# Optimization experiments

Hardware: AMD Instinct MI355X
Metric: run time of the kernel (lower is better)

Reference implementation:

```python
import jax, jax.numpy as jnp
import numpy as np

B, N, E = 16, 4096, 2_000_000
STRENGTH = 1.0
RADIAL_CUTOFF = 3.0
EPS = 1e-8


def setup_inputs() -> dict:
    key = jax.random.key(0)
    k0, k1, k2, k3, k4, k5, k6 = jax.random.split(key, 7)
    relative_coordinates = jax.random.uniform(k0, (B, N, 3), dtype=jnp.float32)
    # well-conditioned unit cells: ~10 Angstrom box with small perturbation
    basis_vectors = 10.0 * jnp.eye(3, dtype=jnp.float32)[None] \
        + 0.3 * jax.random.normal(k1, (B, 3, 3), dtype=jnp.float32)
    src = jax.random.randint(k2, (E,), 0, N)
    dst = jax.random.randint(k3, (E,), 0, N)
    bch = jax.random.randint(k4, (E,), 0, B)
    shifts = 0.5 * jax.random.normal(k5, (E, 3), dtype=jnp.float32)
    raw_scores_X = jax.random.normal(k6, (B, N, 3), dtype=jnp.float32)
    return {
        "relative_coordinates": relative_coordinates,
        "basis_vectors": basis_vectors,
        "shifts": shifts,
        "raw_scores_X": raw_scores_X,
        "src": src,
        "dst": dst,
        "bch": bch,
    }


def reference(relative_coordinates, basis_vectors, shifts, raw_scores_X, src, dst, bch):
    # cartesian positions: rel coords expressed in the basis-vector rows
    pos = jnp.einsum("bni,bij->bnj", relative_coordinates, basis_vectors)  # [B,N,3]
    # per-edge cartesian displacements (gather)
    disp = pos[bch, dst] - pos[bch, src] + shifts  # [E,3]
    r = jnp.linalg.norm(disp, axis=1)  # [E]
    # F(r) prefactor: 2 s (r - r0) / (r + eps)
    prefactor = 2.0 * STRENGTH * (r - RADIAL_CUTOFF) / (r + EPS)
    contributions = prefactor[:, None] * disp  # [E,3]
    # scatter-add edge contributions onto source nodes
    node_idx = N * bch + src
    cart_forces = jax.ops.segment_sum(contributions, node_idx, num_segments=B * N)
    cart_forces = cart_forces.reshape(B, N, 3)
    # back to relative coordinates via reciprocal basis (inverse of basis)
    reciprocal = jnp.linalg.inv(basis_vectors)  # [B,3,3]
    rel_forces = jnp.einsum("bni,bij->bnj", cart_forces, reciprocal)
    # augmented X-score: raw score + repulsive pseudo-force
    return raw_scores_X + rel_forces
```

## Files before the change

kernel.cpp:

```cpp
#include <hip/hip_runtime.h>

#define NBLK 1024
#define NBUK 16
#define NQ   4
#define QSH  10
#define NBUCK (NBUK * NQ)
#define MAXN 4096
#define SCAN_N (NBUCK * NBLK)
#define SCAN_BS 1024
#define MAXPPB 16

__global__ void prep_kernel(const float* __restrict__ rel,
                            const float* __restrict__ basis,
                            const int* __restrict__ src,
                            const int* __restrict__ bch,
                            float4* __restrict__ pos4,
                            int* __restrict__ ghist,
                            int BN, int N, int E, int chunk, int PB) {
    int blk = blockIdx.x, tid = threadIdx.x;
    if (blk < PB) {
        int idx = blk * 256 + tid;
        if (idx < BN) {
            int b = idx / N;
            const float* bm = basis + b * 9;
            float x = rel[idx * 3 + 0], y = rel[idx * 3 + 1], z = rel[idx * 3 + 2];
            float4 p;
            p.x = x * bm[0] + y * bm[3] + z * bm[6];
            p.y = x * bm[1] + y * bm[4] + z * bm[7];
            p.z = x * bm[2] + y * bm[5] + z * bm[8];
            p.w = 0.0f;
            pos4[idx] = p;
        }
        return;
    }
    __shared__ int h[NBUCK];
    int hb = blk - PB;
    if (tid < NBUCK) h[tid] = 0;
    __syncthreads();
    int lo = hb * chunk, hi = min(E, lo + chunk);
    for (int e0 = lo + tid * 8; e0 < hi; e0 += 2048) {
        if (e0 + 7 < hi) {
            int4 bA = *(const int4*)(bch + e0);
            int4 bB = *(const int4*)(bch + e0 + 4);
            int4 sA = *(const int4*)(src + e0);
            int4 sB = *(const int4*)(src + e0 + 4);
            atomicAdd(&h[bA.x * NQ + (sA.x >> QSH)], 1);
            atomicAdd(&h[bA.y * NQ + (sA.y >> QSH)], 1);
            atomicAdd(&h[bA.z * NQ + (sA.z >> QSH)], 1);
            atomicAdd(&h[bA.w * NQ + (sA.w >> QSH)], 1);
            atomicAdd(&h[bB.x * NQ + (sB.x >> QSH)], 1);
            atomicAdd(&h[bB.y * NQ + (sB.y >> QSH)], 1);
            atomicAdd(&h[bB.z * NQ + (sB.z >> QSH)], 1);
            atomicAdd(&h[bB.w * NQ + (sB.w >> QSH)], 1);
        } else {
            for (int e = e0; e < hi; ++e)
                atomicAdd(&h[bch[e] * NQ + (src[e] >> QSH)], 1);
        }
    }
    __syncthreads();
    if (tid < NBUCK) ghist[tid * NBLK + hb] = h[tid];
}

__global__ void scan1_kernel(int* __restrict__ g, int* __restrict__ bsums) {
    __shared__ int tp[256];
    int tid = threadIdx.x;
    int base = blockIdx.x * SCAN_BS + tid * 4;
    int v0 = g[base], v1 = g[base + 1], v2 = g[base + 2], v3 = g[base + 3];
    int s = v0 + v1 + v2 + v3;
    tp[tid] = s;
    for (int off = 1; off < 256; off <<= 1) {
        __syncthreads();
        int t = (tid >= off) ? tp[tid - off] : 0;
        __syncthreads();
        tp[tid] += t;
    }
    __syncthreads();
    int incl = tp[tid];
    int excl = incl - s;
    g[base]     = excl;
    g[base + 1] = excl + v0;
    g[base + 2] = excl + v0 + v1;
    g[base + 3] = excl + v0 + v1 + v2;
    if (tid == 255) bsums[blockIdx.x] = incl;
}

__global__ void scan2_kernel(int* __restrict__ bsums, int n) {
    __shared__ int tp[1024];
    int tid = threadIdx.x;
    int v = (tid < n) ? bsums[tid] : 0;
    tp[tid] = v;
    for (int off = 1; off < 1024; off <<= 1) {
        __syncthreads();
        int t = (tid >= off) ? tp[tid - off] : 0;
        __syncthreads();
        tp[tid] += t;
    }
    __syncthreads();
    if (tid < n) bsums[tid] = tp[tid] - v;
}

__global__ void scatter_kernel(const float* __restrict__ shifts,
                               const int* __restrict__ src,
                               const int* __restrict__ dst,
                               const int* __restrict__ bch,
                               const int* __restrict__ ghist,
                               const int* __restrict__ bsums,
                               float4* __restrict__ recs,
                               int E, int chunk) {
    __shared__ int cur[NBUCK];
    int tid = threadIdx.x, blk = blockIdx.x;
    if (tid < NBUCK) {
        int idx = tid * NBLK + blk;
        cur[tid] = ghist[idx] + bsums[idx >> 10];
    }
    __syncthreads();
    int lo = blk * chunk, hi = min(E, lo + chunk);
    for (int e0 = lo + tid * 8; e0 < hi; e0 += 2048) {
        if (e0 + 7 < hi) {
            int4 sA = *(const int4*)(src + e0);
            int4 sB = *(const int4*)(src + e0 + 4);
            int4 dA = *(const int4*)(dst + e0);
            int4 dB = *(const int4*)(dst + e0 + 4);
            int4 bA = *(const int4*)(bch + e0);
            int4 bB = *(const int4*)(bch + e0 + 4);
            const float4* sh4 = (const float4*)(shifts + (size_t)e0 * 3);
            float4 F0 = sh4[0], F1 = sh4[1], F2 = sh4[2];
            float4 F3 = sh4[3], F4 = sh4[4], F5 = sh4[5];
            int se[8] = {sA.x, sA.y, sA.z, sA.w, sB.x, sB.y, sB.z, sB.w};
            int de[8] = {dA.x, dA.y, dA.z, dA.w, dB.x, dB.y, dB.z, dB.w};
            int be[8] = {bA.x, bA.y, bA.z, bA.w, bB.x, bB.y, bB.z, bB.w};
            float sx[8] = {F0.x, F0.w, F1.z, F2.y, F3.x, F3.w, F4.z, F5.y};
            float sy[8] = {F0.y, F1.x, F1.w, F2.z, F3.y, F4.x, F4.w, F5.z};
            float sz[8] = {F0.z, F1.y, F2.x, F2.w, F3.z, F4.y, F5.x, F5.w};
#pragma unroll
            for (int k = 0; k < 8; ++k) {
                int slot = atomicAdd(&cur[be[k] * NQ + (se[k] >> QSH)], 1);
                float4 rec;
                rec.x = sx[k]; rec.y = sy[k]; rec.z = sz[k];
                rec.w = __int_as_float(se[k] | (de[k] << 12));
                recs[slot] = rec;
            }
        } else {
            for (int e = e0; e < hi; ++e) {
                int slot = atomicAdd(&cur[bch[e] * NQ + (src[e] >> QSH)], 1);
                float4 rec;
                rec.x = shifts[(size_t)e * 3 + 0];
                rec.y = shifts[(size_t)e * 3 + 1];
                rec.z = shifts[(size_t)e * 3 + 2];
                rec.w = __int_as_float(src[e] | (dst[e] << 12));
                recs[slot] = rec;
            }
        }
    }
}

__global__ __launch_bounds__(256, 4)
void accum_kernel(const float4* __restrict__ recs,
                  const float4* __restrict__ pos4,
                  const int* __restrict__ ghist,
                  const int* __restrict__ bsums,
                  float* __restrict__ partials,
                  int E, int N, int PPB) {
    __shared__ float acc[(1 << QSH) * 3];
    int bx = blockIdx.x;
    int bucket = bx / PPB, p = bx - bucket * PPB;
    int b = bucket >> 2, q = bucket & 3;
    int nb = q << QSH;
    int tid = threadIdx.x;
    for (int i = tid * 4; i < (1 << QSH) * 3; i += 1024)
        *(float4*)&acc[i] = make_float4(0.f, 0.f, 0.f, 0.f);
    __syncthreads();
    int g0 = bucket * NBLK;
    int i0 = ghist[g0] + bsums[g0 >> 10];
    int i1 = E;
    if (bucket + 1 < NBUCK) {
        int g1 = (bucket + 1) * NBLK;
        i1 = ghist[g1] + bsums[g1 >> 10];
    }
    const float4* pb = pos4 + (size_t)b * N;
    long long len = (long long)(i1 - i0);
    int lo = i0 + (int)(len * p / PPB);
    int hi = i0 + (int)(len * (p + 1) / PPB);

#define PROC(r)                                                        \
    {                                                                  \
        int u = __float_as_int((r).w);                                 \
        int s_ = u & 4095, d_ = (u >> 12) & 4095;                      \
        float4 P = pb[d_], Q = pb[s_];                                 \
        float dx = P.x - Q.x + (r).x;                                  \
        float dy = P.y - Q.y + (r).y;                                  \
        float dz = P.z - Q.z + (r).z;                                  \
        float rr = sqrtf(dx * dx + dy * dy + dz * dz);                 \
        float pref = 2.0f * (rr - 3.0f) / (rr + 1e-8f);                \
        int nl = s_ - nb;                                              \
        atomicAdd(&acc[nl * 3 + 0], pref * dx);                        \
        atomicAdd(&acc[nl * 3 + 1], pref * dy);                        \
        atomicAdd(&acc[nl * 3 + 2], pref * dz);                        \
    }

    int i = lo + tid;
    for (; i + 768 < hi; i += 1024) {
        float4 r0 = recs[i];
        float4 r1 = recs[i + 256];
        float4 r2 = recs[i + 512];
        float4 r3 = recs[i + 768];
        PROC(r0); PROC(r1); PROC(r2); PROC(r3);
    }
    for (; i < hi; i += 256) {
        float4 r = recs[i];
        PROC(r);
    }
#undef PROC
    __syncthreads();
    float* dstp = partials + (size_t)bx * ((1 << QSH) * 3);
    for (int i2 = tid * 4; i2 < (1 << QSH) * 3; i2 += 1024)
        *(float4*)&dstp[i2] = *(const float4*)&acc[i2];
}

__global__ void final_kernel(const float* __restrict__ partials,
                             const float* __restrict__ basis,
                             const float* __restrict__ raw,
                             float* __restrict__ out,
                             int BN, int N, int PPB) {
    int idx = blockIdx.x * blockDim.x + threadIdx.x;
    if (idx >= BN) return;
    int b = idx / N;
    int n = idx - b * N;
    int q = n >> QSH;
    int nl = n - (q << QSH);
    int bucket = b * NQ + q;
    const int Q3 = (1 << QSH) * 3;
    const float* pp = partials + (size_t)bucket * PPB * Q3 + (size_t)nl * 3;
    float x = 0.f, y = 0.f, z = 0.f;
    for (int p = 0; p < PPB; ++p) {
        x += pp[0]; y += pp[1]; z += pp[2];
        pp += Q3;
    }
    const float* m = basis + b * 9;
    float a00 = m[0], a01 = m[1], a02 = m[2];
    float a10 = m[3], a11 = m[4], a12 = m[5];
    float a20 = m[6], a21 = m[7], a22 = m[8];
    float c00 = a11 * a22 - a12 * a21;
    float c01 = -(a10 * a22 - a12 * a20);
    float c02 = a10 * a21 - a11 * a20;
    float det = a00 * c00 + a01 * c01 + a02 * c02;
    float id = 1.0f / det;
    float rm0 = c00 * id;
    float rm1 = (a02 * a21 - a01 * a22) * id;
    float rm2 = (a01 * a12 - a02 * a11) * id;
    float rm3 = c01 * id;
    float rm4 = (a00 * a22 - a02 * a20) * id;
    float rm5 = (a02 * a10 - a00 * a12) * id;
    float rm6 = c02 * id;
    float rm7 = (a01 * a20 - a00 * a21) * id;
    float rm8 = (a00 * a11 - a01 * a10) * id;
    out[idx * 3 + 0] = raw[idx * 3 + 0] + x * rm0 + y * rm3 + z * rm6;
    out[idx * 3 + 1] = raw[idx * 3 + 1] + x * rm1 + y * rm4 + z * rm7;
    out[idx * 3 + 2] = raw[idx * 3 + 2] + x * rm2 + y * rm5 + z * rm8;
}

__global__ void pos3_kernel(const float* __restrict__ rel,
                            const float* __restrict__ basis,
                            float* __restrict__ pos,
                            int BN, int N) {
    int idx = blockIdx.x * blockDim.x + threadIdx.x;
    if (idx >= BN) return;
    int b = idx / N;
    const float* bm = basis + b * 9;
    float x = rel[idx * 3 + 0], y = rel[idx * 3 + 1], z = rel[idx * 3 + 2];
    pos[idx * 3 + 0] = x * bm[0] + y * bm[3] + z * bm[6];
    pos[idx * 3 + 1] = x * bm[1] + y * bm[4] + z * bm[7];
    pos[idx * 3 + 2] = x * bm[2] + y * bm[5] + z * bm[8];
}

__global__ void inv_kernel(const float* __restrict__ basis,
                           float* __restrict__ recip, int B) {
    int b = blockIdx.x * blockDim.x + threadIdx.x;
    if (b >= B) return;
    const float* m = basis + b * 9;
    float a00 = m[0], a01 = m[1], a02 = m[2];
    float a10 = m[3], a11 = m[4], a12 = m[5];
    float a20 = m[6], a21 = m[7], a22 = m[8];
    float c00 = a11 * a22 - a12 * a21;
    float c01 = -(a10 * a22 - a12 * a20);
    float c02 = a10 * a21 - a11 * a20;
    float det = a00 * c00 + a01 * c01 + a02 * c02;
    float id = 1.0f / det;
    float* r = recip + b * 9;
    r[0] = c00 * id;
    r[1] = (a02 * a21 - a01 * a22) * id;
    r[2] = (a01 * a12 - a02 * a11) * id;
    r[3] = c01 * id;
    r[4] = (a00 * a22 - a02 * a20) * id;
    r[5] = (a02 * a10 - a00 * a12) * id;
    r[6] = c02 * id;
    r[7] = (a01 * a20 - a00 * a21) * id;
    r[8] = (a00 * a11 - a01 * a10) * id;
}

__global__ void edge_kernel_dev(const float* __restrict__ pos,
                                const float* __restrict__ shifts,
                                const int* __restrict__ src,
                                const int* __restrict__ dst,
                                const int* __restrict__ bch,
                                float* __restrict__ cart,
                                int E, int N) {
    int e = blockIdx.x * blockDim.x + threadIdx.x;
    if (e >= E) return;
    int b = bch[e], s = src[e], d = dst[e];
    int base = b * N;
    const float* pd = pos + (size_t)(base + d) * 3;
    const float* ps = pos + (size_t)(base + s) * 3;
    float dx = pd[0] - ps[0] + shifts[(size_t)e * 3 + 0];
    float dy = pd[1] - ps[1] + shifts[(size_t)e * 3 + 1];
    float dz = pd[2] - ps[2] + shifts[(size_t)e * 3 + 2];
    float r = sqrtf(dx * dx + dy * dy + dz * dz);
    float pref = 2.0f * (r - 3.0f) / (r + 1e-8f);
    float* c = cart + (size_t)(base + s) * 3;
    atomicAdd(&c[0], pref * dx);
    atomicAdd(&c[1], pref * dy);
    atomicAdd(&c[2], pref * dz);
}

__global__ void out_kernel(const float* __restrict__ cart,
                           const float* __restrict__ recip,
                           const float* __restrict__ raw,
                           float* __restrict__ out,
                           int BN, int N) {
    int idx = blockIdx.x * blockDim.x + threadIdx.x;
    if (idx >= BN) return;
    int b = idx / N;
    const float* rm = recip + b * 9;
    float x = cart[idx * 3 + 0], y = cart[idx * 3 + 1], z = cart[idx * 3 + 2];
    out[idx * 3 + 0] = raw[idx * 3 + 0] + x * rm[0] + y * rm[3] + z * rm[6];
    out[idx * 3 + 1] = raw[idx * 3 + 1] + x * rm[1] + y * rm[4] + z * rm[7];
    out[idx * 3 + 2] = raw[idx * 3 + 2] + x * rm[2] + y * rm[5] + z * rm[8];
}

extern "C" void kernel_launch(void* const* d_in, const int* in_sizes, int n_in,
                              void* d_out, int out_size, void* d_ws, size_t ws_size,
                              hipStream_t stream) {
    const float* rel    = (const float*)d_in[0];
    const float* basis  = (const float*)d_in[1];
    const float* shifts = (const float*)d_in[2];
    const float* raw    = (const float*)d_in[3];
    const int*   src    = (const int*)d_in[4];
    const int*   dst    = (const int*)d_in[5];
    const int*   bch    = (const int*)d_in[6];

    int B  = in_sizes[1] / 9;
    int BN = in_sizes[0] / 3;
    int N  = BN / B;
    int E  = in_sizes[4];

    char* w = (char*)d_ws;
    float4* recs  = (float4*)w;  w += (size_t)E * 16;
    float4* pos4  = (float4*)w;  w += (size_t)BN * 16;
    int*    ghist = (int*)w;     w += (size_t)SCAN_N * 4;
    int*    bsums = (int*)w;     w += 1024 * 4;
    float*  partials = (float*)w;
    size_t base_bytes = (size_t)(w - (char*)d_ws);

    bool geom_ok = (B >= 1) && (B <= NBUK) && (N >= 4) && (N <= MAXN) &&
                   (BN == B * N) && (E >= 8);
    size_t per_ppb = (size_t)B * NQ * (1 << QSH) * 3 * 4;
    int PPB = 0;
    if (geom_ok && ws_size > base_bytes)
        PPB = (int)((ws_size - base_bytes) / per_ppb);
    if (PPB > MAXPPB) PPB = MAXPPB;

    if (geom_ok && PPB >= 2) {
        int chunk = ((E + NBLK - 1) / NBLK + 7) & ~7;
        int PB = (BN + 255) / 256;
        prep_kernel<<<PB + NBLK, 256, 0, stream>>>(rel, basis, src, bch, pos4, ghist,
                                                   BN, N, E, chunk, PB);
        scan1_kernel<<<SCAN_N / SCAN_BS, 256, 0, stream>>>(ghist, bsums);
        scan2_kernel<<<1, 1024, 0, stream>>>(bsums, SCAN_N / SCAN_BS);
        scatter_kernel<<<NBLK, 256, 0, stream>>>(shifts, src, dst, bch, ghist, bsums,
                                                 recs, E, chunk);
        accum_kernel<<<B * NQ * PPB, 256, 0, stream>>>(recs, pos4, ghist, bsums,
                                                       partials, E, N, PPB);
        final_kernel<<<(BN + 255) / 256, 256, 0, stream>>>(partials, basis, raw,
                                                           (float*)d_out, BN, N, PPB);
    } else {
        float* pos  = (float*)d_ws;
        float* cart = pos + (size_t)BN * 3;
        float* rcp  = cart + (size_t)BN * 3;
        hipMemsetAsync(cart, 0, (size_t)BN * 3 * sizeof(float), stream);
        pos3_kernel<<<(BN + 255) / 256, 256, 0, stream>>>(rel, basis, pos, BN, N);
        inv_kernel<<<1, 64, 0, stream>>>(basis, rcp, B);
        edge_kernel_dev<<<(E + 255) / 256, 256, 0, stream>>>(pos, shifts, src, dst, bch,
                                                             cart, E, N);
        out_kernel<<<(BN + 255) / 256, 256, 0, stream>>>(cart, rcp, raw,
                                                         (float*)d_out, BN, N);
    }
}
```

Baseline: 73.00 us.

## Fold block-sum scan into consumers and fuse final reduction into accum via last-block counter

```diff
diff --git a/kernel.cpp b/kernel.cpp
--- a/kernel.cpp
+++ b/kernel.cpp
@@ -10,12 +10,27 @@
 #define SCAN_BS 1024
 #define MAXPPB 16
 
+__device__ __forceinline__ void scan_bsums(const int* __restrict__ bsums, int* sb, int tid) {
+    if (tid < 64) {
+        int v = bsums[tid];
+        int a = v;
+#pragma unroll
+        for (int off = 1; off < 64; off <<= 1) {
+            int t = __shfl_up(a, off, 64);
+            if (tid >= off) a += t;
+        }
+        sb[tid] = a - v;
+    }
+    __syncthreads();
+}
+
 __global__ void prep_kernel(const float* __restrict__ rel,
                             const float* __restrict__ basis,
                             const int* __restrict__ src,
                             const int* __restrict__ bch,
                             float4* __restrict__ pos4,
                             int* __restrict__ ghist,
+                            int* __restrict__ done,
                             int BN, int N, int E, int chunk, int PB) {
     int blk = blockIdx.x, tid = threadIdx.x;
     if (blk < PB) {
@@ -35,6 +50,7 @@
     }
     __shared__ int h[NBUCK];
     int hb = blk - PB;
+    if (hb == 0 && tid < NBUCK) done[tid] = 0;
     if (tid < NBUCK) h[tid] = 0;
     __syncthreads();
     int lo = hb * chunk, hi = min(E, lo + chunk);
@@ -84,21 +100,6 @@
     if (tid == 255) bsums[blockIdx.x] = incl;
 }
 
-__global__ void scan2_kernel(int* __restrict__ bsums, int n) {
-    __shared__ int tp[1024];
-    int tid = threadIdx.x;
-    int v = (tid < n) ? bsums[tid] : 0;
-    tp[tid] = v;
-    for (int off = 1; off < 1024; off <<= 1) {
-        __syncthreads();
-        int t = (tid >= off) ? tp[tid - off] : 0;
-        __syncthreads();
-        tp[tid] += t;
-    }
-    __syncthreads();
-    if (tid < n) bsums[tid] = tp[tid] - v;
-}
-
 __global__ void scatter_kernel(const float* __restrict__ shifts,
                                const int* __restrict__ src,
                                const int* __restrict__ dst,
@@ -107,12 +108,11 @@
                                const int* __restrict__ bsums,
                                float4* __restrict__ recs,
                                int E, int chunk) {
+    __shared__ int sb[NBUCK];
     __shared__ int cur[NBUCK];
     int tid = threadIdx.x, blk = blockIdx.x;
-    if (tid < NBUCK) {
-        int idx = tid * NBLK + blk;
-        cur[tid] = ghist[idx] + bsums[idx >> 10];
-    }
+    scan_bsums(bsums, sb, tid);
+    if (tid < NBUCK) cur[tid] = ghist[tid * NBLK + blk] + sb[tid];
     __syncthreads();
     int lo = blk * chunk, hi = min(E, lo + chunk);
     for (int e0 = lo + tid * 8; e0 < hi; e0 += 2048) {
@@ -160,23 +160,26 @@
                   const int* __restrict__ ghist,
                   const int* __restrict__ bsums,
                   float* __restrict__ partials,
+                  int* __restrict__ done,
+                  const float* __restrict__ basis,
+                  const float* __restrict__ raw,
+                  float* __restrict__ out,
                   int E, int N, int PPB) {
     __shared__ float acc[(1 << QSH) * 3];
+    __shared__ int sb[NBUCK];
+    __shared__ int lastflag;
     int bx = blockIdx.x;
     int bucket = bx / PPB, p = bx - bucket * PPB;
     int b = bucket >> 2, q = bucket & 3;
     int nb = q << QSH;
     int tid = threadIdx.x;
+    scan_bsums(bsums, sb, tid);
     for (int i = tid * 4; i < (1 << QSH) * 3; i += 1024)
         *(float4*)&acc[i] = make_float4(0.f, 0.f, 0.f, 0.f);
     __syncthreads();
-    int g0 = bucket * NBLK;
-    int i0 = ghist[g0] + bsums[g0 >> 10];
+    int i0 = ghist[bucket * NBLK] + sb[bucket];
     int i1 = E;
-    if (bucket + 1 < NBUCK) {
-        int g1 = (bucket + 1) * NBLK;
-        i1 = ghist[g1] + bsums[g1 >> 10];
-    }
+    if (bucket + 1 < NBUCK) i1 = ghist[(bucket + 1) * NBLK] + sb[bucket + 1];
     const float4* pb = pos4 + (size_t)b * N;
     long long len = (long long)(i1 - i0);
     int lo = i0 + (int)(len * p / PPB);
@@ -212,30 +215,20 @@
     }
 #undef PROC
     __syncthreads();
-    float* dstp = partials + (size_t)bx * ((1 << QSH) * 3);
-    for (int i2 = tid * 4; i2 < (1 << QSH) * 3; i2 += 1024)
+    const int Q3 = (1 << QSH) * 3;
+    float* dstp = partials + (size_t)bx * Q3;
+    for (int i2 = tid * 4; i2 < Q3; i2 += 1024)
         *(float4*)&dstp[i2] = *(const float4*)&acc[i2];
-}
-
-__global__ void final_kernel(const float* __restrict__ partials,
-                             const float* __restrict__ basis,
-                             const float* __restrict__ raw,
-                             float* __restrict__ out,
-                             int BN, int N, int PPB) {
-    int idx = blockIdx.x * blockDim.x + threadIdx.x;
-    if (idx >= BN) return;
-    int b = idx / N;
-    int n = idx - b * N;
-    int q = n >> QSH;
-    int nl = n - (q << QSH);
-    int bucket = b * NQ + q;
-    const int Q3 = (1 << QSH) * 3;
-    const float* pp = partials + (size_t)bucket * PPB * Q3 + (size_t)nl * 3;
-    float x = 0.f, y = 0.f, z = 0.f;
-    for (int p = 0; p < PPB; ++p) {
-        x += pp[0]; y += pp[1]; z += pp[2];
-        pp += Q3;
-    }
+
+    __threadfence();
+    if (tid == 0) {
+        int old = atomicAdd(&done[bucket], 1);
+        lastflag = (old == PPB - 1);
+    }
+    __syncthreads();
+    if (!lastflag) return;
+    __threadfence();
+
     const float* m = basis + b * 9;
     float a00 = m[0], a01 = m[1], a02 = m[2];
     float a10 = m[3], a11 = m[4], a12 = m[5];
@@ -254,9 +247,21 @@
     float rm6 = c02 * id;
     float rm7 = (a01 * a20 - a00 * a21) * id;
     float rm8 = (a00 * a11 - a01 * a10) * id;
-    out[idx * 3 + 0] = raw[idx * 3 + 0] + x * rm0 + y * rm3 + z * rm6;
-    out[idx * 3 + 1] = raw[idx * 3 + 1] + x * rm1 + y * rm4 + z * rm7;
-    out[idx * 3 + 2] = raw[idx * 3 + 2] + x * rm2 + y * rm5 + z * rm8;
+
+    size_t nodebase = (size_t)b * N + nb;
+    const float* pbase = partials + (size_t)bucket * PPB * Q3;
+    for (int f = tid; f < (1 << QSH); f += 256) {
+        float x = 0.f, y = 0.f, z = 0.f;
+        const float* pp = pbase + (size_t)f * 3;
+        for (int p2 = 0; p2 < PPB; ++p2) {
+            x += pp[0]; y += pp[1]; z += pp[2];
+            pp += Q3;
+        }
+        size_t o = (nodebase + f) * 3;
+        out[o + 0] = raw[o + 0] + x * rm0 + y * rm3 + z * rm6;
+        out[o + 1] = raw[o + 1] + x * rm1 + y * rm4 + z * rm7;
+        out[o + 2] = raw[o + 2] + x * rm2 + y * rm5 + z * rm8;
+    }
 }
 
 __global__ void pos3_kernel(const float* __restrict__ rel,
@@ -357,7 +362,8 @@
     float4* recs  = (float4*)w;  w += (size_t)E * 16;
     float4* pos4  = (float4*)w;  w += (size_t)BN * 16;
     int*    ghist = (int*)w;     w += (size_t)SCAN_N * 4;
-    int*    bsums = (int*)w;     w += 1024 * 4;
+    int*    bsums = (int*)w;     w += 64 * 4;
+    int*    done  = (int*)w;     w += 64 * 4;
     float*  partials = (float*)w;
     size_t base_bytes = (size_t)(w - (char*)d_ws);
 
@@ -373,15 +379,13 @@
         int chunk = ((E + NBLK - 1) / NBLK + 7) & ~7;
         int PB = (BN + 255) / 256;
         prep_kernel<<<PB + NBLK, 256, 0, stream>>>(rel, basis, src, bch, pos4, ghist,
-                                                   BN, N, E, chunk, PB);
+                                                   done, BN, N, E, chunk, PB);
         scan1_kernel<<<SCAN_N / SCAN_BS, 256, 0, stream>>>(ghist, bsums);
-        scan2_kernel<<<1, 1024, 0, stream>>>(bsums, SCAN_N / SCAN_BS);
         scatter_kernel<<<NBLK, 256, 0, stream>>>(shifts, src, dst, bch, ghist, bsums,
                                                  recs, E, chunk);
         accum_kernel<<<B * NQ * PPB, 256, 0, stream>>>(recs, pos4, ghist, bsums,
-                                                       partials, E, N, PPB);
-        final_kernel<<<(BN + 255) / 256, 256, 0, stream>>>(partials, basis, raw,
-                                                           (float*)d_out, BN, N, PPB);
+                                                       partials, done, basis, raw,
+                                                       (float*)d_out, E, N, PPB);
     } else {
         float* pos  = (float*)d_ws;
         float* cart = pos + (size_t)BN * 3;
```

After: 207.4 us. 2.84x slower.
